# Optimization experiments

Hardware: AMD Instinct MI355X
Metric: run time of the kernel (lower is better)

## Reference

```python
import jax, jax.numpy as jnp
import numpy as np

B, TZ, TU = 32, 16, 128
E, H, V = 512, 1024, 32000
FREQ_THRES = 4   # cfg.freq_thres: zero out copy prob for most-frequent tokens
LN_EPS = 1e-3


def setup_inputs() -> dict:
    key = jax.random.key(0)
    ks = jax.random.split(key, 16)
    s = lambda k, shape, sc=0.02: jax.random.normal(k, shape, jnp.float32) * sc
    return dict(
        z_enc_out=jax.random.normal(ks[0], (TZ, B, H), jnp.float32),
        pz_proba=jax.nn.softmax(jax.random.normal(ks[1], (TZ, B, V), jnp.float32), axis=-1),
        u_enc_out=jax.random.normal(ks[2], (TU, B, H), jnp.float32),
        m_t_input=jax.random.randint(ks[3], (1, B), 0, V),
        last_hidden=jax.random.normal(ks[4], (1, B, H), jnp.float32),
        emb=s(ks[5], (V, E), 1.0 / np.sqrt(E)),
        Wa_z=s(ks[6], (2 * H, H)), ba_z=jnp.zeros((H,), jnp.float32), v_z=s(ks[7], (H,), 1.0 / np.sqrt(H)),
        Wa_u=s(ks[8], (2 * H, H)), ba_u=jnp.zeros((H,), jnp.float32), v_u=s(ks[9], (H,), 1.0 / np.sqrt(H)),
        W_ih=s(ks[10], (3 * H, E + 2 * H)), W_hh=s(ks[11], (3 * H, H)),
        b_ih=jnp.zeros((3 * H,), jnp.float32), b_hh=jnp.zeros((3 * H,), jnp.float32),
        ln_a=jnp.ones((H,), jnp.float32), ln_b=jnp.zeros((H,), jnp.float32),
        W_proj=s(ks[12], (H, V)), b_proj=jnp.zeros((V,), jnp.float32),
        W_c=s(ks[13], (2 * H, H)), b_c=jnp.zeros((H,), jnp.float32),
        W_v1=s(ks[14], (H, 1)), b_v1=jnp.zeros((1,), jnp.float32),
    )


def _attn(hidden, enc, Wa, ba, v):
    # hidden [1,B,H], enc [T,B,H] -> context [1,B,H]
    hh = jnp.broadcast_to(hidden, enc.shape)                       # [T,B,H]
    energy = jnp.tanh(jnp.concatenate([hh, enc], -1) @ Wa + ba)    # [T,B,H]
    scores = jnp.einsum('tbh,h->bt', energy, v)                    # [B,T]
    w = jax.nn.softmax(scores, axis=1)
    return jnp.einsum('bt,tbh->bh', w, enc)[None]                  # [1,B,H]


def _layernorm(x, a, b):
    mu = jnp.mean(x, axis=-1, keepdims=True)
    sigma = jnp.std(x, axis=-1, keepdims=True, ddof=1)  # torch.std is unbiased
    return (x - mu) / (sigma + LN_EPS) * a + b


def reference(z_enc_out, pz_proba, u_enc_out, m_t_input, last_hidden,
              emb, Wa_z, ba_z, v_z, Wa_u, ba_u, v_u,
              W_ih, W_hh, b_ih, b_hh, ln_a, ln_b,
              W_proj, b_proj, W_c, b_c, W_v1, b_v1):
    m_embed = emb[m_t_input]                                       # [1,B,E]
    z_ctx = _attn(last_hidden, z_enc_out, Wa_z, ba_z, v_z)         # [1,B,H]
    u_ctx = _attn(last_hidden, u_enc_out, Wa_u, ba_u, v_u)         # [1,B,H]
    x = jnp.concatenate([z_ctx, u_ctx, m_embed], -1)[0]            # [B,2H+E]
    h = last_hidden[0]                                             # [B,H]
    # single-step GRU (torch gate order: r, z, n)
    gi = x @ W_ih.T + b_ih
    gh = h @ W_hh.T + b_hh
    ir, iz, inn = jnp.split(gi, 3, axis=-1)
    hr, hz, hn = jnp.split(gh, 3, axis=-1)
    r = jax.nn.sigmoid(ir + hr)
    zg = jax.nn.sigmoid(iz + hz)
    n = jnp.tanh(inn + r * hn)
    h_new = (1.0 - zg) * n + zg * h                                # [B,H]
    gru_out = _layernorm(h_new, ln_a, ln_b)                        # [B,H]
    gen_score = gru_out @ W_proj + b_proj                          # [B,V]
    # tanh-linear copy score over z positions
    g_rep = jnp.broadcast_to(gru_out[None], z_enc_out.shape)       # [Tz,B,H]
    zc = jnp.tanh(jnp.concatenate([z_enc_out, g_rep], -1) @ W_c + b_c)  # [Tz,B,H]
    zc = (zc @ W_v1 + b_v1)[..., 0].T                              # [B,Tz]
    # joint softmax over [gen | copy]
    scores = jax.nn.softmax(jnp.concatenate([gen_score, zc], axis=1), axis=1)
    gen_p, copy_p = scores[:, :V], scores[:, V:]
    copy_v = jnp.einsum('bt,tbv->bv', copy_p, pz_proba)            # mask_prob bmm
    freq_mask = (jnp.arange(V) >= FREQ_THRES).astype(gen_p.dtype)
    proba = gen_p + copy_v * freq_mask
    return proba, h_new[None]
```

## Files before the change

### kernel.cpp

```cpp
#include <hip/hip_runtime.h>
#include <stdint.h>

#define B_ 32
#define TZ_ 16
#define TU_ 128
#define E_ 512
#define H_ 1024
#define V_ 32000
#define X_ 2560
#define H3_ 3072
#define LN_EPS_ 0.001f

typedef unsigned short ushort_t;
typedef ushort_t us4 __attribute__((ext_vector_type(4)));
typedef ushort_t us8 __attribute__((ext_vector_type(8)));
typedef short bf16x8 __attribute__((ext_vector_type(8)));
typedef float f32x4 __attribute__((ext_vector_type(4)));

__device__ __forceinline__ float bf2f(ushort_t u){
  union { unsigned int i; float f; } x; x.i = ((unsigned int)u) << 16; return x.f;
}
__device__ __forceinline__ ushort_t f2b(float f){
  union { float f; unsigned int i; } u; u.f = f;
  unsigned int x = u.i;
  return (ushort_t)((x + 0x7fffu + ((x >> 16) & 1u)) >> 16);
}
__device__ __forceinline__ bool is_bf(const void* lnA){
  return *(const unsigned int*)lnA == 0x3F803F80u;
}
__device__ __forceinline__ float ldg_(const void* p, size_t i, bool isb){
  return isb ? bf2f(((const ushort_t*)p)[i]) : ((const float*)p)[i];
}
__device__ __forceinline__ float sigm(float x){ return 1.0f/(1.0f + __expf(-x)); }
__device__ __forceinline__ float tanh_f(float x){
  float cx = fminf(fmaxf(x, -9.0f), 9.0f);
  float t = __expf(2.0f*cx);
  return (t - 1.0f)/(t + 1.0f);
}

__global__ void k0_init(const void* lh, const void* emb, const int* mt,
                        const void* ba_z, const void* ba_u, const void* b_c,
                        const void* b_ih, const void* b_hh, const void* bpj,
                        const void* lnA,
                        ushort_t* hb, ushort_t* xb, float* hWaZ, float* hWaU,
                        float* sz, float* su, float* gruWc, float* gi, float* gh,
                        float* genscore){
  bool isb = is_bf(lnA);
  int i = blockIdx.x*256 + threadIdx.x;
  if (i < 32768){ hb[i] = f2b(ldg_(lh, i, isb)); return; }
  i -= 32768;
  if (i < 16384){ int b = i >> 9, e = i & 511;
    xb[b*X_ + 2048 + e] = f2b(ldg_(emb, (size_t)(unsigned)mt[b]*E_ + e, isb)); return; }
  i -= 16384;
  if (i < 32768){ hWaZ[i] = ldg_(ba_z, i & 1023, isb); return; }
  i -= 32768;
  if (i < 32768){ hWaU[i] = ldg_(ba_u, i & 1023, isb); return; }
  i -= 32768;
  if (i < 4608){ if (i < 512) sz[i] = 0.f; else su[i-512] = 0.f; return; }
  i -= 4608;
  if (i < 32768){ gruWc[i] = ldg_(b_c, i & 1023, isb); return; }
  i -= 32768;
  if (i < 98304){ gi[i] = ldg_(b_ih, i % H3_, isb); return; }
  i -= 98304;
  if (i < 98304){ gh[i] = ldg_(b_hh, i % H3_, isb); return; }
  i -= 98304;
  if (i < 1024000){
    int b = i / V_;
    int v = i - b*V_;
    genscore[(size_t)b*V_ + v] = ldg_(bpj, v, isb);
  }
}

__global__ void kC_cvt(const void* uenc, const void* zenc, const void* Wih, const void* Whh,
                       const void* lnA,
                       ushort_t* uB, ushort_t* zB, ushort_t* WihB, ushort_t* WhhB){
  bool isb = is_bf(lnA);
  long long i = (long long)(blockIdx.x*256 + threadIdx.x) * 8;
  const long long NU = (long long)TU_*B_*H_;
  const long long NZ = (long long)TZ_*B_*H_;
  const long long NI = (long long)H3_*X_;
  const long long NH = (long long)H3_*H_;
  const void* src; ushort_t* dst;
  if (i < NU){ src = uenc; dst = uB; }
  else if ((i -= NU) < NZ){ src = zenc; dst = zB; }
  else if ((i -= NZ) < NI){ src = Wih; dst = WihB; }
  else if ((i -= NI) < NH){ src = Whh; dst = WhhB; }
  else return;
  if (isb){
    *(us8*)&dst[i] = *(const us8*)((const ushort_t*)src + i);
  } else {
    const float* s = (const float*)src + i;
    float4 a0 = *(const float4*)s, a1 = *(const float4*)(s + 4);
    us8 o;
    o[0]=f2b(a0.x); o[1]=f2b(a0.y); o[2]=f2b(a0.z); o[3]=f2b(a0.w);
    o[4]=f2b(a1.x); o[5]=f2b(a1.y); o[6]=f2b(a1.z); o[7]=f2b(a1.w);
    *(us8*)&dst[i] = o;
  }
}

__global__ void kT_transpose(const void* Wz, const void* Wu, const void* Wc, const void* lnA,
                             ushort_t* tZ, ushort_t* tU, ushort_t* tC,
                             ushort_t* tZt, ushort_t* tUt, ushort_t* tCb){
  bool isb = is_bf(lnA);
  int w = blockIdx.z;
  const void* src = (w==0||w==3)? Wz : (w==1||w==4)? Wu : Wc;
  size_t base = (w==0||w==1||w==5) ? (size_t)H_*H_ : 0;
  ushort_t* dst = (w==0)? tZ : (w==1)? tU : (w==2)? tC : (w==3)? tZt : (w==4)? tUt : tCb;
  __shared__ ushort_t T[64][68];
  int k0 = blockIdx.x*64, j0 = blockIdx.y*64;
  int tx = threadIdx.x & 15, ty = threadIdx.x >> 4;
  if (isb){
    const ushort_t* s = (const ushort_t*)src + base;
    #pragma unroll
    for (int rr=0; rr<4; ++rr){
      int row = ty + rr*16;
      *(us4*)&T[row][tx*4] = *(const us4*)&s[(size_t)(k0+row)*H_ + j0 + tx*4];
    }
  } else {
    const float* s = (const float*)src + base;
    #pragma unroll
    for (int rr=0; rr<4; ++rr){
      int row = ty + rr*16;
      #pragma unroll
      for (int c=0;c<4;c++)
        T[row][tx*4+c] = f2b(s[(size_t)(k0+row)*H_ + j0 + tx*4 + c]);
    }
  }
  __syncthreads();
  #pragma unroll
  for (int rr=0; rr<4; ++rr){
    int row = ty + rr*16;
    us4 o;
    o[0]=T[tx*4+0][row]; o[1]=T[tx*4+1][row]; o[2]=T[tx*4+2][row]; o[3]=T[tx*4+3][row];
    *(us4*)&dst[(size_t)(j0+row)*H_ + k0 + tx*4] = o;
  }
}

__global__ __launch_bounds__(256) void kg_mfma(const ushort_t* Ab0, const ushort_t* Ab1,
                                               const ushort_t* W0, const ushort_t* W1,
                                               float* out0, float* out1, int N){
  const ushort_t* Ab = blockIdx.z ? Ab1 : Ab0;
  const ushort_t* WT = blockIdx.z ? W1 : W0;
  float* out = blockIdx.z ? out1 : out0;
  int j0 = blockIdx.x*128;
  int kchunk = H_ / gridDim.y;
  int kb = blockIdx.y*kchunk;
  __shared__ ushort_t Bs[128*32];
  int tid = threadIdx.x, wid = tid >> 6, lane = tid & 63;
  int q = lane >> 4, n = lane & 15;
  int rrow = tid >> 2, t4 = tid & 3;
  f32x4 acc[2][2];
  #pragma unroll
  for (int r=0;r<2;r++)
    #pragma unroll
    for (int c=0;c<2;c++)
      #pragma unroll
      for (int e=0;e<4;e++) acc[r][c][e] = 0.f;

  for (int kt = 0; kt < kchunk; kt += 32){
    int k = kb + kt;
    __syncthreads();
    #pragma unroll
    for (int p=0;p<2;p++){
      const ushort_t* srcB = WT + (size_t)(j0 + p*64 + rrow)*H_ + k + t4*8;
      __builtin_amdgcn_global_load_lds(srcB, &Bs[(p*64 + wid*16)*32], 16, 0, 0);
    }
    __syncthreads();
    bf16x8 af[2], bfr[2];
    #pragma unroll
    for (int r=0;r<2;r++) af[r] = *(const bf16x8*)&Ab[(size_t)(r*16 + n)*H_ + k + q*8];
    #pragma unroll
    for (int c=0;c<2;c++) bfr[c] = *(const bf16x8*)&Bs[(wid*32 + c*16 + n)*32 + q*8];
    #pragma unroll
    for (int r=0;r<2;r++)
      #pragma unroll
      for (int c=0;c<2;c++)
        acc[r][c] = __builtin_amdgcn_mfma_f32_16x16x32_bf16(af[r], bfr[c], acc[r][c], 0, 0, 0);
  }
  #pragma unroll
  for (int r=0;r<2;r++)
    #pragma unroll
    for (int c=0;c<2;c++)
      #pragma unroll
      for (int i=0;i<4;i++){
        int b = r*16 + q*4 + i;
        int j = j0 + wid*32 + c*16 + n;
        unsafeAtomicAdd(&out[(size_t)b*N + j], acc[r][c][i]);
      }
}

__global__ __launch_bounds__(256) void k2_mfma(const ushort_t* Ab, const ushort_t* WB,
                                               float* out, int K, int kchunk){
  int j0 = blockIdx.x*128;
  int kb = blockIdx.y*kchunk;
  __shared__ ushort_t Bs[128*32];
  int tid = threadIdx.x, wid = tid >> 6, lane = tid & 63;
  int q = lane >> 4, n = lane & 15;
  int rrow = tid >> 2, t4 = tid & 3;
  f32x4 acc[2][2];
  #pragma unroll
  for (int r=0;r<2;r++)
    #pragma unroll
    for (int c=0;c<2;c++)
      #pragma unroll
      for (int e=0;e<4;e++) acc[r][c][e] = 0.f;

  for (int kt = 0; kt < kchunk; kt += 32){
    int k = kb + kt;
    __syncthreads();
    #pragma unroll
    for (int p=0;p<2;p++){
      const ushort_t* srcB = WB + (size_t)(j0 + p*64 + rrow)*K + k + t4*8;
      __builtin_amdgcn_global_load_lds(srcB, &Bs[(p*64 + wid*16)*32], 16, 0, 0);
    }
    __syncthreads();
    bf16x8 af[2], bfr[2];
    #pragma unroll
    for (int r=0;r<2;r++) af[r] = *(const bf16x8*)&Ab[(size_t)(r*16 + n)*K + k + q*8];
    #pragma unroll
    for (int c=0;c<2;c++) bfr[c] = *(const bf16x8*)&Bs[(wid*32 + c*16 + n)*32 + q*8];
    #pragma unroll
    for (int r=0;r<2;r++)
      #pragma unroll
      for (int c=0;c<2;c++)
        acc[r][c] = __builtin_amdgcn_mfma_f32_16x16x32_bf16(af[r], bfr[c], acc[r][c], 0, 0, 0);
  }
  #pragma unroll
  for (int r=0;r<2;r++)
    #pragma unroll
    for (int c=0;c<2;c++)
      #pragma unroll
      for (int i=0;i<4;i++){
        int b = r*16 + q*4 + i;
        int j = j0 + wid*32 + c*16 + n;
        unsafeAtomicAdd(&out[(size_t)b*H3_ + j], acc[r][c][i]);
      }
}

__global__ __launch_bounds__(256) void k6p_mfma(const ushort_t* grub, const void* Wp,
                                                const void* lnA, float* genscore){
  bool isb = is_bf(lnA);
  int j0 = blockIdx.x*128;
  int kchunk = H_ / gridDim.y;
  int kb = blockIdx.y*kchunk;
  __shared__ float Ts[32][129];
  int tid = threadIdx.x, wid = tid >> 6, lane = tid & 63;
  int q = lane >> 4, n = lane & 15;
  int lrow = tid >> 3, lcol = (tid & 7)*16;
  f32x4 acc[2][2];
  #pragma unroll
  for (int r=0;r<2;r++)
    #pragma unroll
    for (int c=0;c<2;c++)
      #pragma unroll
      for (int e=0;e<4;e++) acc[r][c][e] = 0.f;

  for (int kt = 0; kt < kchunk; kt += 32){
    int k = kb + kt;
    __syncthreads();
    if (isb){
      const ushort_t* s = (const ushort_t*)Wp + (size_t)(k + lrow)*V_ + j0 + lcol;
      us8 a0 = *(const us8*)s;
      us8 a1 = *(const us8*)(s + 8);
      #pragma unroll
      for (int e=0;e<8;e++){ Ts[lrow][lcol+e] = bf2f(a0[e]); Ts[lrow][lcol+8+e] = bf2f(a1[e]); }
    } else {
      const float* s = (const float*)Wp + (size_t)(k + lrow)*V_ + j0 + lcol;
      float4 f0 = *(const float4*)s,     f1 = *(const float4*)(s+4);
      float4 f2 = *(const float4*)(s+8), f3 = *(const float4*)(s+12);
      *(float4*)&Ts[lrow][lcol]    = f0;
      *(float4*)&Ts[lrow][lcol+4]  = f1;
      *(float4*)&Ts[lrow][lcol+8]  = f2;
      *(float4*)&Ts[lrow][lcol+12] = f3;
    }
    __syncthreads();
    bf16x8 af[2], bfr[2];
    #pragma unroll
    for (int r=0;r<2;r++) af[r] = *(const bf16x8*)&grub[(size_t)(r*16 + n)*H_ + k + q*8];
    #pragma unroll
    for (int c=0;c<2;c++){
      int vl = wid*32 + c*16 + n;
      us8 o;
      #pragma unroll
      for (int e=0;e<8;e++) o[e] = f2b(Ts[q*8 + e][vl]);
      bfr[c] = *(bf16x8*)&o;
    }
    #pragma unroll
    for (int r=0;r<2;r++)
      #pragma unroll
      for (int c=0;c<2;c++)
        acc[r][c] = __builtin_amdgcn_mfma_f32_16x16x32_bf16(af[r], bfr[c], acc[r][c], 0, 0, 0);
  }
  #pragma unroll
  for (int r=0;r<2;r++)
    #pragma unroll
    for (int c=0;c<2;c++)
      #pragma unroll
      for (int i=0;i<4;i++){
        int b = r*16 + q*4 + i;
        int v = j0 + wid*32 + c*16 + n;
        unsafeAtomicAdd(&genscore[(size_t)b*V_ + v], acc[r][c][i]);
      }
}

__global__ __launch_bounds__(256) void k3_mfma(
    const ushort_t* uB, const ushort_t* zB,
    const ushort_t* tU, const ushort_t* tZ, const ushort_t* tC,
    const float* hWaU, const float* hWaZ,
    const void* v_u, const void* v_z, const void* lnA,
    float* su, float* sz, float* zcpre)
{
  bool isb = is_bf(lnA);
  int which = blockIdx.z;
  int bx = blockIdx.x, nt = blockIdx.y;
  int mt;
  const ushort_t* A; const ushort_t* BT;
  if (which == 0){ A = uB; BT = tU; mt = bx; }
  else {
    int lo = (which==1) ? 8 : 12;
    if (bx < lo || bx >= lo+4) return;
    mt = bx - lo;
    A = zB; BT = (which==1) ? tZ : tC;
  }
  __shared__ ushort_t As[128*32];
  __shared__ ushort_t Bs[64*32];
  int tid = threadIdx.x;
  int wid = tid >> 6, lane = tid & 63;
  int q = lane >> 4, n = lane & 15;
  int wm = wid & 1, wn = wid >> 1;
  int r0 = mt*128, j0 = nt*64;
  f32x4 acc[4][2];
  #pragma unroll
  for (int a=0;a<4;a++)
    #pragma unroll
    for (int c=0;c<2;c++)
      #pragma unroll
      for (int e=0;e<4;e++) acc[a][c][e] = 0.f;

  int rrow = tid >> 2, t4 = tid & 3;

  for (int kt = 0; kt < 32; ++kt){
    __syncthreads();
    #pragma unroll
    for (int p=0;p<2;p++){
      const ushort_t* srcA = A + (size_t)(r0 + p*64 + rrow)*H_ + kt*32 + t4*8;
      __builtin_amdgcn_global_load_lds(srcA, &As[(p*64 + wid*16)*32], 16, 0, 0);
    }
    {
      const ushort_t* srcB = BT + (size_t)(j0 + rrow)*H_ + kt*32 + t4*8;
      __builtin_amdgcn_global_load_lds(srcB, &Bs[(wid*16)*32], 16, 0, 0);
    }
    __syncthreads();
    bf16x8 af[4], bfr[2];
    #pragma unroll
    for (int f=0;f<4;f++) af[f] = *(const bf16x8*)&As[(wm*64 + f*16 + n)*32 + q*8];
    #pragma unroll
    for (int f=0;f<2;f++) bfr[f] = *(const bf16x8*)&Bs[(wn*32 + f*16 + n)*32 + q*8];
    #pragma unroll
    for (int fr=0;fr<4;fr++)
      #pragma unroll
      for (int fn=0;fn<2;fn++)
        acc[fr][fn] = __builtin_amdgcn_mfma_f32_16x16x32_bf16(af[fr], bfr[fn], acc[fr][fn], 0, 0, 0);
  }

  if (which < 2){
    const float* pre = (which==0) ? hWaU : hWaZ;
    const void* vv = (which==0) ? v_u : v_z;
    float* score = (which==0) ? su : sz;
    float s[4][4];
    #pragma unroll
    for (int fr=0;fr<4;fr++)
      #pragma unroll
      for (int i=0;i<4;i++) s[fr][i]=0.f;
    #pragma unroll
    for (int fr=0;fr<4;fr++){
      #pragma unroll
      for (int fn=0;fn<2;fn++){
        int j  = j0 + wn*32 + fn*16 + n;
        float vj = ldg_(vv, j, isb);
        #pragma unroll
        for (int i=0;i<4;i++){
          int rl = wm*64 + fr*16 + q*4 + i;
          int b  = rl & 31;
          s[fr][i] += tanh_f(acc[fr][fn][i] + pre[b*H_ + j]) * vj;
        }
      }
    }
    #pragma unroll
    for (int fr=0;fr<4;fr++)
      #pragma unroll
      for (int i=0;i<4;i++){
        float t = s[fr][i];
        t += __shfl_xor(t, 1);
        t += __shfl_xor(t, 2);
        t += __shfl_xor(t, 4);
        t += __shfl_xor(t, 8);
        if (n == 0){
          int rl = wm*64 + fr*16 + q*4 + i;
          unsafeAtomicAdd(&score[r0 + rl], t);
        }
      }
  } else {
    #pragma unroll
    for (int fr=0;fr<4;fr++)
      #pragma unroll
      for (int fn=0;fn<2;fn++)
        #pragma unroll
        for (int i=0;i<4;i++){
          int rl = wm*64 + fr*16 + q*4 + i;
          int jl = wn*32 + fn*16 + n;
          zcpre[(size_t)(r0 + rl)*H_ + j0 + jl] = acc[fr][fn][i];
        }
  }
}

__global__ void k4_ctx(const float* sz, const float* su,
                       const void* zenc, const void* uenc, const void* lnA, ushort_t* xb){
  bool isb = is_bf(lnA);
  int jc = blockIdx.x, b = blockIdx.y, which = blockIdx.z;
  int T = which ? TU_ : TZ_;
  const float* sc = which ? su : sz;
  const void* enc = which ? uenc : zenc;
  __shared__ float red[256];
  __shared__ float w[TU_];
  int tid = threadIdx.x;
  float v = (tid < T) ? sc[tid*B_ + b] : -1e30f;
  red[tid] = v; __syncthreads();
  for (int s=128; s>0; s>>=1){ if (tid < s) red[tid] = fmaxf(red[tid], red[tid+s]); __syncthreads(); }
  float m = red[0]; __syncthreads();
  float e = (tid < T) ? __expf(v - m) : 0.f;
  red[tid] = e; __syncthreads();
  for (int s=128; s>0; s>>=1){ if (tid < s) red[tid] += red[tid+s]; __syncthreads(); }
  float S = red[0]; __syncthreads();
  if (tid < T) w[tid] = e / S;
  __syncthreads();
  int j = jc*256 + tid;
  float acc = 0.f;
  #pragma unroll 4
  for (int t=0; t<T; ++t) acc = fmaf(w[t], ldg_(enc, (size_t)(t*B_ + b)*H_ + j, isb), acc);
  xb[b*X_ + which*H_ + j] = f2b(acc);
}

__global__ __launch_bounds__(1024) void k5_gru(const float* gi, const float* gh,
                       const void* lh, const void* ln_a, const void* ln_b,
                       ushort_t* grub, float* hout){
  bool isb = is_bf(ln_a);
  int b = blockIdx.x, tid = threadIdx.x;
  __shared__ float red[1024];
  int j = tid;
  float ir = gi[(size_t)b*H3_ + j], iz = gi[(size_t)b*H3_ + 1024 + j], inn = gi[(size_t)b*H3_ + 2048 + j];
  float hr = gh[(size_t)b*H3_ + j], hz = gh[(size_t)b*H3_ + 1024 + j], hn = gh[(size_t)b*H3_ + 2048 + j];
  float hv = ldg_(lh, b*H_ + j, isb);
  float r  = sigm(ir + hr);
  float zg = sigm(iz + hz);
  float nn = tanh_f(inn + r*hn);
  float h2 = (1.f - zg)*nn + zg*hv;
  hout[b*H_ + j] = h2;
  red[tid] = h2; __syncthreads();
  for (int s=512;s>0;s>>=1){ if(tid<s) red[tid]+=red[tid+s]; __syncthreads(); }
  float mu = red[0] / 1024.f; __syncthreads();
  red[tid] = h2*h2; __syncthreads();
  for (int s=512;s>0;s>>=1){ if(tid<s) red[tid]+=red[tid+s]; __syncthreads(); }
  float var = (red[0] - 1024.f*mu*mu) / 1023.f;
  float sg = sqrtf(fmaxf(var, 0.f));
  float inv = 1.f/(sg + LN_EPS_);
  float g = (h2 - mu)*inv*ldg_(ln_a, j, isb) + ldg_(ln_b, j, isb);
  grub[b*H_ + j] = f2b(g);
}

__global__ void k7_zc(const float* zcpre, const float* gruWc, const void* Wv1,
                      const void* b_v1, const void* lnA, float* zc){
  bool isb = is_bf(lnA);
  int r = blockIdx.x, b = r & 31, tid = threadIdx.x;
  __shared__ float red[256];
  float s = 0.f;
  #pragma unroll
  for (int jj=0;jj<4;jj++){
    int j = tid + jj*256;
    float e = tanh_f(zcpre[(size_t)r*H_ + j] + gruWc[b*H_ + j]);
    s = fmaf(e, ldg_(Wv1, j, isb), s);
  }
  red[tid] = s; __syncthreads();
  for (int st=128;st>0;st>>=1){ if(tid<st) red[tid]+=red[tid+st]; __syncthreads(); }
  if (tid==0) zc[r] = red[0] + ldg_(b_v1, 0, isb);
}

__global__ void k8a(const float* genscore, float* statpart){
  int v = blockIdx.x*256 + threadIdx.x;
  int b = blockIdx.y, tid = threadIdx.x;
  __shared__ float red[256];
  float g = genscore[(size_t)b*V_ + v];
  red[tid] = g; __syncthreads();
  for (int s=128;s>0;s>>=1){ if(tid<s) red[tid]=fmaxf(red[tid],red[tid+s]); __syncthreads(); }
  float m = red[0]; __syncthreads();
  float e = __expf(g - m);
  red[tid] = e; __syncthreads();
  for (int s=128;s>0;s>>=1){ if(tid<s) red[tid]+=red[tid+s]; __syncthreads(); }
  if (tid==0){ statpart[(b*125 + blockIdx.x)*2] = m; statpart[(b*125 + blockIdx.x)*2+1] = red[0]; }
}

__global__ void k8b(const float* statpart, const float* zc, float* stats, float* copyp){
  int b = blockIdx.x, tid = threadIdx.x;
  __shared__ float red[128];
  float m = -1e30f, s = 0.f;
  if (tid < 125){ m = statpart[(b*125 + tid)*2]; s = statpart[(b*125 + tid)*2 + 1]; }
  float zv = (tid < 16) ? zc[tid*B_ + b] : -1e30f;
  red[tid] = fmaxf(m, zv); __syncthreads();
  for (int st=64;st>0;st>>=1){ if(tid<st) red[tid]=fmaxf(red[tid],red[tid+st]); __syncthreads(); }
  float M = red[0]; __syncthreads();
  float zp = (tid < 125) ? s*__expf(m - M) : 0.f;
  if (tid < 16) zp += __expf(zv - M);
  red[tid] = zp; __syncthreads();
  for (int st=64;st>0;st>>=1){ if(tid<st) red[tid]+=red[tid+st]; __syncthreads(); }
  float invZ = 1.f/red[0];
  if (tid < 16) copyp[b*16 + tid] = __expf(zv - M)*invZ;
  if (tid == 0){ stats[b*2] = M; stats[b*2+1] = invZ; }
}

__global__ void k8c(const float* genscore, const float* stats, const float* copyp,
                    const void* pz, const void* lnA, float* out){
  bool isb = is_bf(lnA);
  int v = blockIdx.x*256 + threadIdx.x;
  int b = blockIdx.y;
  float M = stats[b*2], invZ = stats[b*2+1];
  float p = __expf(genscore[(size_t)b*V_ + v] - M)*invZ;
  if (v >= 4){
    float cv = 0.f;
    if (isb){
      const ushort_t* pzp = (const ushort_t*)pz;
      #pragma unroll
      for (int t=0;t<16;t++)
        cv = fmaf(copyp[b*16 + t], bf2f(pzp[(size_t)(t*B_ + b)*V_ + v]), cv);
    } else {
      const float* pzp = (const float*)pz;
      #pragma unroll
      for (int t=0;t<16;t++)
        cv = fmaf(copyp[b*16 + t], pzp[(size_t)(t*B_ + b)*V_ + v], cv);
    }
    p += cv;
  }
  out[(size_t)b*V_ + v] = p;
}

extern "C" void kernel_launch(void* const* d_in, const int* in_sizes, int n_in,
                              void* d_out, int out_size, void* d_ws, size_t ws_size,
                              hipStream_t stream){
  const void* z_enc = d_in[0];
  const void* pz    = d_in[1];
  const void* u_enc = d_in[2];
  const int*  m_t   = (const int*)d_in[3];
  const void* lh    = d_in[4];
  const void* emb   = d_in[5];
  const void* Wa_z  = d_in[6];
  const void* ba_z  = d_in[7];
  const void* v_z   = d_in[8];
  const void* Wa_u  = d_in[9];
  const void* ba_u  = d_in[10];
  const void* v_u   = d_in[11];
  const void* W_ih  = d_in[12];
  const void* W_hh  = d_in[13];
  const void* b_ih  = d_in[14];
  const void* b_hh  = d_in[15];
  const void* ln_a  = d_in[16];
  const void* ln_b  = d_in[17];
  const void* W_proj= d_in[18];
  const void* b_proj= d_in[19];
  const void* W_c   = d_in[20];
  const void* b_c   = d_in[21];
  const void* W_v1  = d_in[22];
  const void* b_v1  = d_in[23];

  float* wsf = (float*)d_ws;
  size_t o = 0;
  auto alloc = [&](size_t n){ float* p = wsf + o; o += n; return p; };
  float* hWaZ  = alloc(B_*H_);
  float* hWaU  = alloc(B_*H_);
  float* sz    = alloc(TZ_*B_);
  float* su    = alloc(TU_*B_);
  float* gruWc = alloc(B_*H_);
  float* zcpre = alloc((size_t)TZ_*B_*H_);
  float* zcv   = alloc(TZ_*B_);
  float* gi    = alloc((size_t)B_*H3_);
  float* gh    = alloc((size_t)B_*H3_);
  float* genscore = alloc((size_t)B_*V_);
  float* statpart = alloc(B_*125*2);
  float* stats = alloc(B_*2);
  float* copyp = alloc(B_*TZ_);
  o = (o + 7) & ~(size_t)7;
  ushort_t* wT = (ushort_t*)(wsf + o);
  ushort_t* tZ  = wT;
  ushort_t* tU  = wT + (size_t)H_*H_;
  ushort_t* tC  = wT + (size_t)2*H_*H_;
  ushort_t* tZt = wT + (size_t)3*H_*H_;
  ushort_t* tUt = wT + (size_t)4*H_*H_;
  ushort_t* tCb = wT + (size_t)5*H_*H_;
  o += (size_t)6*H_*H_/2;
  ushort_t* uB = (ushort_t*)(wsf + o);
  o += (size_t)TU_*B_*H_/2;
  ushort_t* zB = (ushort_t*)(wsf + o);
  o += (size_t)TZ_*B_*H_/2;
  ushort_t* WihB = (ushort_t*)(wsf + o);
  o += (size_t)H3_*X_/2;
  ushort_t* WhhB = (ushort_t*)(wsf + o);
  o += (size_t)H3_*H_/2;
  ushort_t* xb = (ushort_t*)(wsf + o);
  o += (size_t)B_*X_/2;
  ushort_t* hb = (ushort_t*)(wsf + o);
  o += (size_t)B_*H_/2;
  ushort_t* grub = (ushort_t*)(wsf + o);
  o += (size_t)B_*H_/2;
  float* outp = (float*)d_out;
  float* hout = outp + (size_t)B_*V_;

  k0_init<<<5362, 256, 0, stream>>>(lh, emb, m_t, ba_z, ba_u, b_c, b_ih, b_hh, b_proj, ln_a,
                                    hb, xb, hWaZ, hWaU, sz, su, gruWc, gi, gh, genscore);
  kC_cvt<<<7680, 256, 0, stream>>>(u_enc, z_enc, W_ih, W_hh, ln_a, uB, zB, WihB, WhhB);
  kT_transpose<<<dim3(16,16,6), 256, 0, stream>>>(Wa_z, Wa_u, W_c, ln_a, tZ, tU, tC, tZt, tUt, tCb);
  kg_mfma<<<dim3(8,8,2), 256, 0, stream>>>(hb, hb, tZt, tUt, hWaZ, hWaU, H_);
  k2_mfma<<<dim3(24,16), 256, 0, stream>>>(hb, WhhB, gh, H_, 64);
  k3_mfma<<<dim3(32,16,3), 256, 0, stream>>>(uB, zB, tU, tZ, tC, hWaU, hWaZ, v_u, v_z, ln_a, su, sz, zcpre);
  k4_ctx<<<dim3(4,32,2), 256, 0, stream>>>(sz, su, z_enc, u_enc, ln_a, xb);
  k2_mfma<<<dim3(24,20), 256, 0, stream>>>(xb, WihB, gi, X_, 128);
  k5_gru<<<32, 1024, 0, stream>>>(gi, gh, lh, ln_a, ln_b, grub, hout);
  kg_mfma<<<dim3(8,8,1), 256, 0, stream>>>(grub, grub, tCb, tCb, gruWc, gruWc, H_);
  k7_zc<<<512, 256, 0, stream>>>(zcpre, gruWc, W_v1, b_v1, ln_a, zcv);
  k6p_mfma<<<dim3(250,8), 256, 0, stream>>>(grub, W_proj, ln_a, genscore);
  k8a<<<dim3(125,32), 256, 0, stream>>>(genscore, statpart);
  k8b<<<32, 128, 0, stream>>>(statpart, zcv, stats, copyp);
  k8c<<<dim3(125,32), 256, 0, stream>>>(genscore, stats, copyp, pz, ln_a, outp);
}
```

Before: 465.9 us.

## Drop GRU weight pre-conversion; convert W_ih/W_hh on the fly in GEMM

The separate conversion kernel no longer writes bf16 copies of W_ih and W_hh. The GRU GEMMs now read the original weights, stage them in shared memory as fp32 and round them to bf16 when building MFMA fragments. The u/z encoder conversion is folded into the init kernel, and the output-projection grid's second dimension is halved. This removes one kernel launch and a full write-then-read pass over the GRU weights. In exchange the GEMMs load twice as many bytes when inputs are fp32 and spend more ALU and LDS time converting values.

```diff
diff --git a/kernel.cpp b/kernel.cpp
--- a/kernel.cpp
+++ b/kernel.cpp
@@ -41,10 +41,11 @@
 __global__ void k0_init(const void* lh, const void* emb, const int* mt,
                         const void* ba_z, const void* ba_u, const void* b_c,
                         const void* b_ih, const void* b_hh, const void* bpj,
+                        const void* uenc, const void* zenc,
                         const void* lnA,
                         ushort_t* hb, ushort_t* xb, float* hWaZ, float* hWaU,
                         float* sz, float* su, float* gruWc, float* gi, float* gh,
-                        float* genscore){
+                        float* genscore, ushort_t* uB, ushort_t* zB){
   bool isb = is_bf(lnA);
   int i = blockIdx.x*256 + threadIdx.x;
   if (i < 32768){ hb[i] = f2b(ldg_(lh, i, isb)); return; }
@@ -68,33 +69,27 @@
     int b = i / V_;
     int v = i - b*V_;
     genscore[(size_t)b*V_ + v] = ldg_(bpj, v, isb);
-  }
-}
-
-__global__ void kC_cvt(const void* uenc, const void* zenc, const void* Wih, const void* Whh,
-                       const void* lnA,
-                       ushort_t* uB, ushort_t* zB, ushort_t* WihB, ushort_t* WhhB){
-  bool isb = is_bf(lnA);
-  long long i = (long long)(blockIdx.x*256 + threadIdx.x) * 8;
-  const long long NU = (long long)TU_*B_*H_;
-  const long long NZ = (long long)TZ_*B_*H_;
-  const long long NI = (long long)H3_*X_;
-  const long long NH = (long long)H3_*H_;
-  const void* src; ushort_t* dst;
-  if (i < NU){ src = uenc; dst = uB; }
-  else if ((i -= NU) < NZ){ src = zenc; dst = zB; }
-  else if ((i -= NZ) < NI){ src = Wih; dst = WihB; }
-  else if ((i -= NI) < NH){ src = Whh; dst = WhhB; }
-  else return;
-  if (isb){
-    *(us8*)&dst[i] = *(const us8*)((const ushort_t*)src + i);
-  } else {
-    const float* s = (const float*)src + i;
-    float4 a0 = *(const float4*)s, a1 = *(const float4*)(s + 4);
-    us8 o;
-    o[0]=f2b(a0.x); o[1]=f2b(a0.y); o[2]=f2b(a0.z); o[3]=f2b(a0.w);
-    o[4]=f2b(a1.x); o[5]=f2b(a1.y); o[6]=f2b(a1.z); o[7]=f2b(a1.w);
-    *(us8*)&dst[i] = o;
+    return;
+  }
+  i -= 1024000;
+  {
+    long long e8 = (long long)i * 8;
+    const long long NU = (long long)TU_*B_*H_;
+    const long long NZ = (long long)TZ_*B_*H_;
+    const void* src; ushort_t* dst; long long off;
+    if (e8 < NU){ src = uenc; dst = uB; off = e8; }
+    else if (e8 < NU + NZ){ src = zenc; dst = zB; off = e8 - NU; }
+    else return;
+    if (isb){
+      *(us8*)&dst[off] = *(const us8*)((const ushort_t*)src + off);
+    } else {
+      const float* s = (const float*)src + off;
+      float4 a0 = *(const float4*)s, a1 = *(const float4*)(s + 4);
+      us8 o;
+      o[0]=f2b(a0.x); o[1]=f2b(a0.y); o[2]=f2b(a0.z); o[3]=f2b(a0.w);
+      o[4]=f2b(a1.x); o[5]=f2b(a1.y); o[6]=f2b(a1.z); o[7]=f2b(a1.w);
+      *(us8*)&dst[off] = o;
+    }
   }
 }
 
@@ -189,14 +184,15 @@
       }
 }
 
-__global__ __launch_bounds__(256) void k2_mfma(const ushort_t* Ab, const ushort_t* WB,
-                                               float* out, int K, int kchunk){
+__global__ __launch_bounds__(256) void k2f_mfma(const ushort_t* Ab, const void* W,
+                                                const void* lnA, float* out, int K, int kchunk){
+  bool isb = is_bf(lnA);
   int j0 = blockIdx.x*128;
   int kb = blockIdx.y*kchunk;
-  __shared__ ushort_t Bs[128*32];
+  __shared__ float Ws[128][33];
   int tid = threadIdx.x, wid = tid >> 6, lane = tid & 63;
   int q = lane >> 4, n = lane & 15;
-  int rrow = tid >> 2, t4 = tid & 3;
+  int srow = tid >> 1, scol = (tid & 1)*16;
   f32x4 acc[2][2];
   #pragma unroll
   for (int r=0;r<2;r++)
@@ -208,17 +204,33 @@
   for (int kt = 0; kt < kchunk; kt += 32){
     int k = kb + kt;
     __syncthreads();
-    #pragma unroll
-    for (int p=0;p<2;p++){
-      const ushort_t* srcB = WB + (size_t)(j0 + p*64 + rrow)*K + k + t4*8;
-      __builtin_amdgcn_global_load_lds(srcB, &Bs[(p*64 + wid*16)*32], 16, 0, 0);
+    if (isb){
+      const ushort_t* s = (const ushort_t*)W + (size_t)(j0 + srow)*K + k + scol;
+      us8 a0 = *(const us8*)s;
+      us8 a1 = *(const us8*)(s + 8);
+      #pragma unroll
+      for (int e=0;e<8;e++){ Ws[srow][scol+e] = bf2f(a0[e]); Ws[srow][scol+8+e] = bf2f(a1[e]); }
+    } else {
+      const float* s = (const float*)W + (size_t)(j0 + srow)*K + k + scol;
+      float4 f0 = *(const float4*)s,     f1 = *(const float4*)(s+4);
+      float4 f2 = *(const float4*)(s+8), f3 = *(const float4*)(s+12);
+      *(float4*)&Ws[srow][scol]    = f0;
+      *(float4*)&Ws[srow][scol+4]  = f1;
+      *(float4*)&Ws[srow][scol+8]  = f2;
+      *(float4*)&Ws[srow][scol+12] = f3;
     }
     __syncthreads();
     bf16x8 af[2], bfr[2];
     #pragma unroll
     for (int r=0;r<2;r++) af[r] = *(const bf16x8*)&Ab[(size_t)(r*16 + n)*K + k + q*8];
     #pragma unroll
-    for (int c=0;c<2;c++) bfr[c] = *(const bf16x8*)&Bs[(wid*32 + c*16 + n)*32 + q*8];
+    for (int c=0;c<2;c++){
+      int jl = wid*32 + c*16 + n;
+      us8 o;
+      #pragma unroll
+      for (int e=0;e<8;e++) o[e] = f2b(Ws[jl][q*8 + e]);
+      bfr[c] = *(bf16x8*)&o;
+    }
     #pragma unroll
     for (int r=0;r<2;r++)
       #pragma unroll
@@ -599,10 +611,6 @@
   o += (size_t)TU_*B_*H_/2;
   ushort_t* zB = (ushort_t*)(wsf + o);
   o += (size_t)TZ_*B_*H_/2;
-  ushort_t* WihB = (ushort_t*)(wsf + o);
-  o += (size_t)H3_*X_/2;
-  ushort_t* WhhB = (ushort_t*)(wsf + o);
-  o += (size_t)H3_*H_/2;
   ushort_t* xb = (ushort_t*)(wsf + o);
   o += (size_t)B_*X_/2;
   ushort_t* hb = (ushort_t*)(wsf + o);
@@ -612,19 +620,20 @@
   float* outp = (float*)d_out;
   float* hout = outp + (size_t)B_*V_;
 
-  k0_init<<<5362, 256, 0, stream>>>(lh, emb, m_t, ba_z, ba_u, b_c, b_ih, b_hh, b_proj, ln_a,
-                                    hb, xb, hWaZ, hWaU, sz, su, gruWc, gi, gh, genscore);
-  kC_cvt<<<7680, 256, 0, stream>>>(u_enc, z_enc, W_ih, W_hh, ln_a, uB, zB, WihB, WhhB);
+  k0_init<<<7666, 256, 0, stream>>>(lh, emb, m_t, ba_z, ba_u, b_c, b_ih, b_hh, b_proj,
+                                    u_enc, z_enc, ln_a,
+                                    hb, xb, hWaZ, hWaU, sz, su, gruWc, gi, gh, genscore,
+                                    uB, zB);
   kT_transpose<<<dim3(16,16,6), 256, 0, stream>>>(Wa_z, Wa_u, W_c, ln_a, tZ, tU, tC, tZt, tUt, tCb);
   kg_mfma<<<dim3(8,8,2), 256, 0, stream>>>(hb, hb, tZt, tUt, hWaZ, hWaU, H_);
-  k2_mfma<<<dim3(24,16), 256, 0, stream>>>(hb, WhhB, gh, H_, 64);
+  k2f_mfma<<<dim3(24,16), 256, 0, stream>>>(hb, W_hh, ln_a, gh, H_, 64);
   k3_mfma<<<dim3(32,16,3), 256, 0, stream>>>(uB, zB, tU, tZ, tC, hWaU, hWaZ, v_u, v_z, ln_a, su, sz, zcpre);
   k4_ctx<<<dim3(4,32,2), 256, 0, stream>>>(sz, su, z_enc, u_enc, ln_a, xb);
-  k2_mfma<<<dim3(24,20), 256, 0, stream>>>(xb, WihB, gi, X_, 128);
+  k2f_mfma<<<dim3(24,20), 256, 0, stream>>>(xb, W_ih, ln_a, gi, X_, 128);
   k5_gru<<<32, 1024, 0, stream>>>(gi, gh, lh, ln_a, ln_b, grub, hout);
   kg_mfma<<<dim3(8,8,1), 256, 0, stream>>>(grub, grub, tCb, tCb, gruWc, gruWc, H_);
   k7_zc<<<512, 256, 0, stream>>>(zcpre, gruWc, W_v1, b_v1, ln_a, zcv);
-  k6p_mfma<<<dim3(250,8), 256, 0, stream>>>(grub, W_proj, ln_a, genscore);
+  k6p_mfma<<<dim3(250,4), 256, 0, stream>>>(grub, W_proj, ln_a, genscore);
   k8a<<<dim3(125,32), 256, 0, stream>>>(genscore, statpart);
   k8b<<<32, 128, 0, stream>>>(statpart, zcv, stats, copyp);
   k8c<<<dim3(125,32), 256, 0, stream>>>(genscore, stats, copyp, pz, ln_a, outp);
```

After: 456.8 us, median of 2. -2.0%, faster.
